# Kernel optimization log

Measured on AMD Instinct MI355X. Metric: run time of the kernel, lower is better.

Reference implementation:

```python
import jax, jax.numpy as jnp
import numpy as np

B, T, HID, H, DH, K = 2, 1024, 1024, 16, 64, 4
ROPE_BASE = 10000.0
EPS = 1e-6


def _causal_dwconv(x, w, b):
    # x: (B, T, C); w: (C, 1, K) depthwise; causal left-pad K-1, then SiLU
    xc = jnp.transpose(x, (0, 2, 1))  # (B, C, T)
    y = jax.lax.conv_general_dilated(
        xc, w, window_strides=(1,), padding=[(K - 1, 0)],
        dimension_numbers=('NCH', 'OIH', 'NCH'), feature_group_count=xc.shape[1])
    y = y + b[None, :, None]
    return jax.nn.silu(jnp.transpose(y, (0, 2, 1)))


def _rope(x, cos, sin):
    # x: (B, T, H, D); cos/sin: (T, D) with emb = cat(freqs, freqs)
    c = cos[None, :, None, :]
    s = sin[None, :, None, :]
    x1, x2 = x[..., ::2], x[..., 1::2]
    return jnp.concatenate(
        [x1 * c[..., ::2] - x2 * s[..., ::2],
         x1 * s[..., ::2] + x2 * c[..., ::2]], axis=-1)


def _delta_rule(q, k, v, alpha, beta, D_param):
    # q,k,v: (B,T,H,DH); alpha,beta: (B,T,H)
    # S_t = alpha_t * (I - beta_t k_t k_t^T) S_{t-1} + beta_t k_t v_t^T
    # o_t  = q_t^T S_t-1-style readout + D * (q.k) * v   (matches torch einsum 'bhd,bhde->bhe')
    qs = jnp.moveaxis(q, 1, 0).astype(jnp.float32)  # (T,B,H,DH)
    ks = jnp.moveaxis(k, 1, 0).astype(jnp.float32)
    vs = jnp.moveaxis(v, 1, 0).astype(jnp.float32)
    als = jnp.moveaxis(alpha, 1, 0).astype(jnp.float32)  # (T,B,H)
    bes = jnp.moveaxis(beta, 1, 0).astype(jnp.float32)

    def step(S, inp):
        qt, kt, vt, at, bt = inp
        ot = jnp.einsum('bhd,bhde->bhe', qt, S)
        ot = ot + D_param[None, :, None] * jnp.sum(qt * kt, -1, keepdims=True) * vt
        kS = jnp.einsum('bhd,bhde->bhe', kt, S)  # k^T S
        at_ = at[..., None, None]
        bt_ = bt[..., None, None]
        S_new = at_ * (S - bt_ * kt[..., :, None] * kS[..., None, :]) \
                + bt_ * kt[..., :, None] * vt[..., None, :]
        return S_new, ot

    S0 = jnp.zeros((q.shape[0], H, DH, DH), jnp.float32)
    _, outs = jax.lax.scan(step, S0, (qs, ks, vs, als, bes))
    return jnp.moveaxis(outs, 0, 1)  # (B,T,H,DH)


def _forward(x, Wq, Wk, Wv, Wg, Wo, bw, bb, gkw, gkb,
             qcw, qcb, kcw, kcb, vcw, vcb, A_log, D_param, dt_bias, onorm_w):
    Bb, Tt, _ = x.shape
    q = _causal_dwconv(x @ Wq, qcw, qcb).reshape(Bb, Tt, H, DH)
    k = _causal_dwconv(x @ Wk, kcw, kcb).reshape(Bb, Tt, H, DH)
    v = _causal_dwconv(x @ Wv, vcw, vcb).reshape(Bb, Tt, H, DH)

    # RoPE (computed on the fly, fp32)
    t = jnp.arange(Tt, dtype=jnp.float32)
    inv_freq = 1.0 / (ROPE_BASE ** (jnp.arange(0, DH, 2, dtype=jnp.float32) / DH))
    freqs = jnp.outer(t, inv_freq)
    emb = jnp.concatenate([freqs, freqs], -1)
    cos, sin = jnp.cos(emb), jnp.sin(emb)
    q = _rope(q, cos, sin)
    k = _rope(k, cos, sin)

    # L2-normalize q/k (delta-net stability, NOT softmax)
    q = q * jax.lax.rsqrt(jnp.sum(q * q, -1, keepdims=True) + EPS)
    k = k * jax.lax.rsqrt(jnp.sum(k * k, -1, keepdims=True) + EPS)

    beta = jax.nn.sigmoid(x @ bw + bb)  # (B,T,H) writing strength
    alpha = jnp.exp(-jnp.exp(A_log) * jax.nn.softplus(x @ gkw + gkb + dt_bias))  # (B,T,H) decay

    o = _delta_rule(q, k, v, alpha, beta, D_param)  # (B,T,H,DH)

    # gated RMSNorm output: g * silu(RMSNorm(o))
    g = (x @ Wg).reshape(Bb, Tt, H, DH)
    on = o * jax.lax.rsqrt(jnp.mean(o * o, -1, keepdims=True) + EPS) * onorm_w
    o = g * jax.nn.silu(on)
    return o.reshape(Bb, Tt, H * DH) @ Wo


def setup_inputs() -> dict:
    key = jax.random.key(0)
    ks = jax.random.split(key, 20)
    w = lambda i, shape, s=0.02: (jax.random.normal(ks[i], shape, jnp.float32) * s)
    return {
        'x': jax.random.normal(ks[0], (B, T, HID), jnp.float32),
        'Wq': w(1, (HID, H * DH)), 'Wk': w(2, (HID, H * DH)),
        'Wv': w(3, (HID, H * DH)), 'Wg': w(4, (HID, H * DH)),
        'Wo': w(5, (H * DH, HID)),
        'bw': w(6, (HID, H)), 'bb': jnp.zeros((H,), jnp.float32),
        'gkw': w(7, (HID, H)), 'gkb': jnp.zeros((H,), jnp.float32),
        'qcw': w(8, (H * DH, 1, K), 0.3), 'qcb': jnp.zeros((H * DH,), jnp.float32),
        'kcw': w(9, (H * DH, 1, K), 0.3), 'kcb': jnp.zeros((H * DH,), jnp.float32),
        'vcw': w(10, (H * DH, 1, K), 0.3), 'vcb': jnp.zeros((H * DH,), jnp.float32),
        'A_log': jnp.log(jax.random.uniform(ks[11], (H,), jnp.float32, 1.0, 16.0)),
        'D_param': jnp.ones((H,), jnp.float32),
        'dt_bias': jax.random.uniform(ks[12], (H,), jnp.float32, -0.01, 0.01),
        'onorm_w': jnp.ones((DH,), jnp.float32),
    }


def reference(x, Wq, Wk, Wv, Wg, Wo, bw, bb, gkw, gkb,
              qcw, qcb, kcw, kcb, vcw, vcb, A_log, D_param, dt_bias, onorm_w):
    return _forward(x, Wq, Wk, Wv, Wg, Wo, bw, bb, gkw, gkb,
                    qcw, qcb, kcw, kcb, vcw, vcb, A_log, D_param, dt_bias, onorm_w)
```

## Files before the change

kernel.cpp:

```cpp
#include <hip/hip_runtime.h>
#include <hip/hip_bf16.h>
#include <cstdint>

#define T_LEN 1024
#define HIDN  1024
#define NH    16
#define DHD   64

typedef __bf16 bf16x8 __attribute__((ext_vector_type(8)));
typedef float  f32x4  __attribute__((ext_vector_type(4)));

__global__ __launch_bounds__(256) void k_tobf16_split(const float* __restrict__ in,
                                                      __bf16* __restrict__ hi,
                                                      __bf16* __restrict__ lo, int n8) {
  int i = blockIdx.x * 256 + threadIdx.x;
  if (i >= n8) return;
  const float4* p = (const float4*)in + (size_t)i * 2;
  float4 a = p[0], b = p[1];
  float v[8] = {a.x, a.y, a.z, a.w, b.x, b.y, b.z, b.w};
  union { __bf16 h[8]; uint4 u; } ph, pl;
#pragma unroll
  for (int j = 0; j < 8; j++) {
    __bf16 h = (__bf16)v[j];
    ph.h[j] = h;
    pl.h[j] = (__bf16)(v[j] - (float)h);
  }
  ((uint4*)hi)[i] = ph.u;
  ((uint4*)lo)[i] = pl.u;
}

__global__ __launch_bounds__(256) void k_transp_split(
    const float* __restrict__ W0, const float* __restrict__ W1,
    const float* __restrict__ W2, const float* __restrict__ W3,
    const float* __restrict__ W4,
    __bf16* __restrict__ H0, __bf16* __restrict__ H1, __bf16* __restrict__ H2,
    __bf16* __restrict__ H3, __bf16* __restrict__ H4,
    __bf16* __restrict__ L0, __bf16* __restrict__ L1, __bf16* __restrict__ L2,
    __bf16* __restrict__ L3, __bf16* __restrict__ L4) {
  const float* W; __bf16* Th; __bf16* Tl;
  switch (blockIdx.z) {
    case 0: W = W0; Th = H0; Tl = L0; break;
    case 1: W = W1; Th = H1; Tl = L1; break;
    case 2: W = W2; Th = H2; Tl = L2; break;
    case 3: W = W3; Th = H3; Tl = L3; break;
    default: W = W4; Th = H4; Tl = L4; break;
  }
  __shared__ float tile[64][65];
  int tid = threadIdx.x;
  int r0 = tid >> 4;
  int c0 = (tid & 15) * 4;
  int kbase = blockIdx.y * 64, nbase = blockIdx.x * 64;
#pragma unroll
  for (int rr = 0; rr < 4; rr++) {
    int r = r0 + rr * 16;
    float4 v = *(const float4*)(W + (size_t)(kbase + r) * 1024 + nbase + c0);
    tile[r][c0 + 0] = v.x; tile[r][c0 + 1] = v.y;
    tile[r][c0 + 2] = v.z; tile[r][c0 + 3] = v.w;
  }
  __syncthreads();
#pragma unroll
  for (int rr = 0; rr < 4; rr++) {
    int n = r0 + rr * 16;
    union { __bf16 h[4]; unsigned long long u; } ph, pl;
#pragma unroll
    for (int j = 0; j < 4; j++) {
      float v = tile[c0 + j][n];
      __bf16 h = (__bf16)v;
      ph.h[j] = h;
      pl.h[j] = (__bf16)(v - (float)h);
    }
    *(unsigned long long*)(Th + (size_t)(nbase + n) * 1024 + kbase + c0) = ph.u;
    *(unsigned long long*)(Tl + (size_t)(nbase + n) * 1024 + kbase + c0) = pl.u;
  }
}

#define LDT 40
__global__ __launch_bounds__(256) void k_gemm3(
    const __bf16* __restrict__ Ah, const __bf16* __restrict__ Al,
    const __bf16* __restrict__ Bh0, const __bf16* __restrict__ Bh1,
    const __bf16* __restrict__ Bh2, const __bf16* __restrict__ Bh3,
    const __bf16* __restrict__ Bl0, const __bf16* __restrict__ Bl1,
    const __bf16* __restrict__ Bl2, const __bf16* __restrict__ Bl3,
    float* __restrict__ C0, float* __restrict__ C1,
    float* __restrict__ C2, float* __restrict__ C3,
    int Kdim, int Ncols) {
  const __bf16* Bh; const __bf16* Bl; float* C;
  switch (blockIdx.z) {
    case 0: Bh = Bh0; Bl = Bl0; C = C0; break;
    case 1: Bh = Bh1; Bl = Bl1; C = C1; break;
    case 2: Bh = Bh2; Bl = Bl2; C = C2; break;
    default: Bh = Bh3; Bl = Bl3; C = C3; break;
  }
  __shared__ __bf16 Ash[128 * LDT];
  __shared__ __bf16 Asl[128 * LDT];
  __shared__ __bf16 Bsh[128 * LDT];
  __shared__ __bf16 Bsl[128 * LDT];
  const int tid = threadIdx.x;
  const int lane = tid & 63;
  const int wave = tid >> 6;
  const int wr = wave >> 1, wc = wave & 1;
  const int rowA0 = blockIdx.y * 128;
  const int colB0 = blockIdx.x * 128;
  const int sseg = tid & 3;
  const int srow0 = tid >> 2;
  const int srow1 = srow0 + 64;

  f32x4 acc[4][4] = {};

  for (int k0 = 0; k0 < Kdim; k0 += 32) {
    size_t a0 = (size_t)(rowA0 + srow0) * Kdim + k0 + sseg * 8;
    size_t a1 = (size_t)(rowA0 + srow1) * Kdim + k0 + sseg * 8;
    size_t b0 = (size_t)(colB0 + srow0) * Kdim + k0 + sseg * 8;
    size_t b1 = (size_t)(colB0 + srow1) * Kdim + k0 + sseg * 8;
    uint4 rah0 = *(const uint4*)(Ah + a0);
    uint4 rah1 = *(const uint4*)(Ah + a1);
    uint4 ral0 = *(const uint4*)(Al + a0);
    uint4 ral1 = *(const uint4*)(Al + a1);
    uint4 rbh0 = *(const uint4*)(Bh + b0);
    uint4 rbh1 = *(const uint4*)(Bh + b1);
    uint4 rbl0 = *(const uint4*)(Bl + b0);
    uint4 rbl1 = *(const uint4*)(Bl + b1);
    __syncthreads();
    *(uint4*)&Ash[srow0 * LDT + sseg * 8] = rah0;
    *(uint4*)&Ash[srow1 * LDT + sseg * 8] = rah1;
    *(uint4*)&Asl[srow0 * LDT + sseg * 8] = ral0;
    *(uint4*)&Asl[srow1 * LDT + sseg * 8] = ral1;
    *(uint4*)&Bsh[srow0 * LDT + sseg * 8] = rbh0;
    *(uint4*)&Bsh[srow1 * LDT + sseg * 8] = rbh1;
    *(uint4*)&Bsl[srow0 * LDT + sseg * 8] = rbl0;
    *(uint4*)&Bsl[srow1 * LDT + sseg * 8] = rbl1;
    __syncthreads();
    bf16x8 afh[4], afl[4], bfh[4], bfl[4];
#pragma unroll
    for (int mi = 0; mi < 4; mi++) {
      int off = (wr * 64 + mi * 16 + (lane & 15)) * LDT + (lane >> 4) * 8;
      afh[mi] = *(const bf16x8*)&Ash[off];
      afl[mi] = *(const bf16x8*)&Asl[off];
    }
#pragma unroll
    for (int ni = 0; ni < 4; ni++) {
      int off = (wc * 64 + ni * 16 + (lane & 15)) * LDT + (lane >> 4) * 8;
      bfh[ni] = *(const bf16x8*)&Bsh[off];
      bfl[ni] = *(const bf16x8*)&Bsl[off];
    }
#pragma unroll
    for (int mi = 0; mi < 4; mi++)
#pragma unroll
      for (int ni = 0; ni < 4; ni++) {
        acc[mi][ni] = __builtin_amdgcn_mfma_f32_16x16x32_bf16(afh[mi], bfh[ni], acc[mi][ni], 0, 0, 0);
        acc[mi][ni] = __builtin_amdgcn_mfma_f32_16x16x32_bf16(afl[mi], bfh[ni], acc[mi][ni], 0, 0, 0);
        acc[mi][ni] = __builtin_amdgcn_mfma_f32_16x16x32_bf16(afh[mi], bfl[ni], acc[mi][ni], 0, 0, 0);
      }
  }
#pragma unroll
  for (int mi = 0; mi < 4; mi++)
#pragma unroll
    for (int ni = 0; ni < 4; ni++) {
      int col = colB0 + wc * 64 + ni * 16 + (lane & 15);
#pragma unroll
      for (int r = 0; r < 4; r++) {
        int row = rowA0 + wr * 64 + mi * 16 + (lane >> 4) * 4 + r;
        C[(size_t)row * Ncols + col] = acc[mi][ni][r];
      }
    }
}

__global__ __launch_bounds__(256) void k_gates(
    const float* __restrict__ x, const float* __restrict__ bw,
    const float* __restrict__ bb, const float* __restrict__ gkw,
    const float* __restrict__ gkb, const float* __restrict__ A_log,
    const float* __restrict__ dt_bias,
    float* __restrict__ alphaB, float* __restrict__ betaB) {
  const int bt = blockIdx.x;
  const int tid = threadIdx.x;
  const int h = tid & 15;
  const int chunk = tid >> 4;
  const float* xr = x + (size_t)bt * HIDN;
  float d1 = 0.f, d2 = 0.f;
#pragma unroll 8
  for (int j = 0; j < 64; j++) {
    int k = chunk * 64 + j;
    float xv = xr[k];
    d1 += xv * bw[k * 16 + h];
    d2 += xv * gkw[k * 16 + h];
  }
  __shared__ float p1[16][16], p2[16][16];
  p1[chunk][h] = d1; p2[chunk][h] = d2;
  __syncthreads();
  if (tid < 16) {
    float s1 = 0.f, s2 = 0.f;
#pragma unroll
    for (int c = 0; c < 16; c++) { s1 += p1[c][tid]; s2 += p2[c][tid]; }
    float beta = 1.f / (1.f + expf(-(s1 + bb[tid])));
    float z = s2 + gkb[tid] + dt_bias[tid];
    float sp = fmaxf(z, 0.f) + log1pf(expf(-fabsf(z)));
    float alpha = expf(-expf(A_log[tid]) * sp);
    alphaB[(size_t)bt * 16 + tid] = alpha;
    betaB[(size_t)bt * 16 + tid] = beta;
  }
}

__global__ __launch_bounds__(256) void k_rope_table(float* __restrict__ ct,
                                                    float* __restrict__ st) {
  int idx = blockIdx.x * 256 + threadIdx.x;
  if (idx >= T_LEN * 32) return;
  int t = idx >> 5, i = idx & 31;
  int m = 2 * (i & 15);
  float f = expf(-(float)m * (9.210340371976184f / 32.f));
  float ang = (float)t * f;
  ct[idx] = cosf(ang);
  st[idx] = sinf(ang);
}

__global__ __launch_bounds__(256) void k_conv(
    const float* __restrict__ in0, const float* __restrict__ in1,
    const float* __restrict__ in2,
    const float* __restrict__ w0, const float* __restrict__ w1,
    const float* __restrict__ w2,
    const float* __restrict__ b0, const float* __restrict__ b1,
    const float* __restrict__ b2,
    float* __restrict__ o0, float* __restrict__ o1, float* __restrict__ o2) {
  const int tensor = blockIdx.y;
  const float* in; const float* w; const float* bias; float* out;
  switch (tensor) {
    case 0: in = in0; w = w0; bias = b0; out = o0; break;
    case 1: in = in1; w = w1; bias = b1; out = o1; break;
    default: in = in2; w = w2; bias = b2; out = o2; break;
  }
  int idx = blockIdx.x * 256 + threadIdx.x;
  int c = idx & 1023;
  int bt = idx >> 10;
  int t = bt & 1023, b = bt >> 10;
  float4 wc4 = *(const float4*)(w + (size_t)c * 4);
  const float* col = in + ((size_t)b * 1024) * 1024 + c;
  float xm3 = (t >= 3) ? col[(size_t)(t - 3) * 1024] : 0.f;
  float xm2 = (t >= 2) ? col[(size_t)(t - 2) * 1024] : 0.f;
  float xm1 = (t >= 1) ? col[(size_t)(t - 1) * 1024] : 0.f;
  float x0 = col[(size_t)t * 1024];
  float acc = bias[c] + wc4.x * xm3 + wc4.y * xm2 + wc4.z * xm1 + wc4.w * x0;
  float y = acc / (1.f + expf(-acc));
  if (tensor < 2) {
    out[(size_t)bt * 1024 + c] = y;
  } else {
    int h = c >> 6, d = c & 63;
    out[(((size_t)(b * 16 + h)) * 1024 + t) * 64 + d] = y;
  }
}

__global__ __launch_bounds__(256) void k_ropenorm(
    const float* __restrict__ qc, const float* __restrict__ kc,
    const float* __restrict__ ct, const float* __restrict__ st,
    const float* __restrict__ alphaB, const float* __restrict__ betaB,
    const float* __restrict__ Dp,
    float* __restrict__ qr, float* __restrict__ kr, float4* __restrict__ aux) {
  int widx = blockIdx.x * 4 + (threadIdx.x >> 6);
  int lane = threadIdx.x & 63;
  int h = widx & 15;
  int bt = widx >> 4;
  int t = bt & 1023, b = bt >> 10;
  const float* qrow = qc + (size_t)bt * 1024 + h * 64;
  const float* krow = kc + (size_t)bt * 1024 + h * 64;
  int i = lane & 31;
  float cv = ct[t * 32 + i], sv = st[t * 32 + i];
  float q1 = qrow[2 * i], q2 = qrow[2 * i + 1];
  float k1 = krow[2 * i], k2 = krow[2 * i + 1];
  float qo = (lane < 32) ? (q1 * cv - q2 * sv) : (q1 * sv + q2 * cv);
  float ko = (lane < 32) ? (k1 * cv - k2 * sv) : (k1 * sv + k2 * cv);
  float qs = qo * qo, ks2 = ko * ko;
#pragma unroll
  for (int m = 1; m < 64; m <<= 1) { qs += __shfl_xor(qs, m); ks2 += __shfl_xor(ks2, m); }
  float qn = qo * rsqrtf(qs + 1e-6f);
  float kn = ko * rsqrtf(ks2 + 1e-6f);
  float dq = qn * kn;
#pragma unroll
  for (int m = 1; m < 64; m <<= 1) dq += __shfl_xor(dq, m);
  size_t obase = ((size_t)(b * 16 + h) * 1024 + t) * 64;
  qr[obase + lane] = qn;
  kr[obase + lane] = kn;
  if (lane == 0) {
    float alpha = alphaB[(size_t)bt * 16 + h];
    float beta = betaB[(size_t)bt * 16 + h];
    aux[(size_t)(b * 16 + h) * 1024 + t] = make_float4(alpha, beta, alpha * beta, Dp[h] * dq);
  }
}

__global__ __launch_bounds__(128) void k_scanA(
    const float* __restrict__ qr, const float* __restrict__ kr,
    const float* __restrict__ vr, const float4* __restrict__ aux,
    float* __restrict__ O1, float* __restrict__ AcF,
    float* __restrict__ BcTF, float* __restrict__ QeffF,
    float* __restrict__ gcF) {
  const int bid = blockIdx.x;
  const int bh = bid >> 4, c = bid & 15;
  const int t0 = c * 64;
  const int tid = threadIdx.x;
  const int w = tid >> 6, lane = tid & 63;
  const float* qB = qr + (size_t)bh * 65536 + (size_t)t0 * 64;
  const float* kB = kr + (size_t)bh * 65536 + (size_t)t0 * 64;
  const float* vB = vr + (size_t)bh * 65536 + (size_t)t0 * 64;
  const float4* auxB = aux + (size_t)bh * T_LEN + t0;

  __shared__ __bf16 q_b[64 * 72];
  __shared__ __bf16 k_b[64 * 72];
  __shared__ __bf16 kT_b[64 * 72];
  __shared__ __bf16 C_b[64 * 72];
  __shared__ __bf16 U0T[64 * 72];
  __shared__ __bf16 WT[64 * 72];
  __shared__ float  vS[64 * 64];
  __shared__ float  MTf[64 * 68];
  __shared__ float  lgS[64], pvS[64], beS[64], awS[64], enS[64];

  if (w == 0) {
    float4 a4 = auxB[lane];
    float lg = logf(a4.x);
#pragma unroll
    for (int off = 1; off < 64; off <<= 1) {
      float tv = __shfl_up(lg, off);
      if (lane >= off) lg += tv;
    }
    float pv = __shfl_up(lg, 1);
    if (lane == 0) pv = 0.f;
    float lgTot = __shfl(lg, 63);
    lgS[lane] = lg; pvS[lane] = pv; beS[lane] = a4.y; awS[lane] = a4.w;
    enS[lane] = expf(lgTot - lg);
    if (lane == 0) gcF[bid] = expf(lgTot);
  }
#pragma unroll
  for (int p = 0; p < 4; p++) {
    int s = p * 128 + tid;
    int row = s >> 3, col8 = s & 7;
    const float* gq = qB + (size_t)row * 64 + col8 * 8;
    const float* gk = kB + (size_t)row * 64 + col8 * 8;
    const float* gv = vB + (size_t)row * 64 + col8 * 8;
    float4 q0 = *(const float4*)gq, q1 = *(const float4*)(gq + 4);
    float4 k0 = *(const float4*)gk, k1 = *(const float4*)(gk + 4);
    float4 v0 = *(const float4*)gv, v1 = *(const float4*)(gv + 4);
    union { __bf16 h[8]; uint4 u; } pq, pk;
    pq.h[0] = (__bf16)q0.x; pq.h[1] = (__bf16)q0.y; pq.h[2] = (__bf16)q0.z; pq.h[3] = (__bf16)q0.w;
    pq.h[4] = (__bf16)q1.x; pq.h[5] = (__bf16)q1.y; pq.h[6] = (__bf16)q1.z; pq.h[7] = (__bf16)q1.w;
    pk.h[0] = (__bf16)k0.x; pk.h[1] = (__bf16)k0.y; pk.h[2] = (__bf16)k0.z; pk.h[3] = (__bf16)k0.w;
    pk.h[4] = (__bf16)k1.x; pk.h[5] = (__bf16)k1.y; pk.h[6] = (__bf16)k1.z; pk.h[7] = (__bf16)k1.w;
    *(uint4*)&q_b[row * 72 + col8 * 8] = pq.u;
    *(uint4*)&k_b[row * 72 + col8 * 8] = pk.u;
    *(float4*)&vS[row * 64 + col8 * 8] = v0;
    *(float4*)&vS[row * 64 + col8 * 8 + 4] = v1;
  }
  __syncthreads();

#pragma unroll
  for (int mm = 0; mm < 2; mm++) {
    int mi = w * 2 + mm;
#pragma unroll
    for (int ni = 0; ni < 4; ni++) {
      f32x4 akk = {0.f, 0.f, 0.f, 0.f};
      f32x4 aqk = {0.f, 0.f, 0.f, 0.f};
#pragma unroll
      for (int ks = 0; ks < 2; ks++) {
        bf16x8 fa_k = *(const bf16x8*)&k_b[(mi * 16 + (lane & 15)) * 72 + ks * 32 + (lane >> 4) * 8];
        bf16x8 fa_q = *(const bf16x8*)&q_b[(mi * 16 + (lane & 15)) * 72 + ks * 32 + (lane >> 4) * 8];
        bf16x8 fb_k = *(const bf16x8*)&k_b[(ni * 16 + (lane & 15)) * 72 + ks * 32 + (lane >> 4) * 8];
        akk = __builtin_amdgcn_mfma_f32_16x16x32_bf16(fa_k, fb_k, akk, 0, 0, 0);
        aqk = __builtin_amdgcn_mfma_f32_16x16x32_bf16(fa_q, fb_k, aqk, 0, 0, 0);
      }
#pragma unroll
      for (int r = 0; r < 4; r++) {
        int row = mi * 16 + (lane >> 4) * 4 + r;
        int col = ni * 16 + (lane & 15);
        float mt = 0.f, cv = 0.f;
        if (row > col) {
          mt = beS[row] * expf(lgS[row] - lgS[col]) * akk[r];
          cv = expf(pvS[row] - lgS[col]) * aqk[r];
        }
        MTf[col * 68 + row] = mt;
        C_b[row * 72 + col] = (__bf16)cv;
      }
    }
  }
  __syncthreads();

  if (w == 1) {
#pragma unroll
    for (int t8 = 0; t8 < 8; t8++) {
      union { __bf16 h[8]; uint4 u; } pt;
#pragma unroll
      for (int q = 0; q < 8; q++) {
        int t = t8 * 8 + q;
        pt.h[q] = (__bf16)((float)k_b[t * 72 + lane] * enS[t]);
      }
      *(uint4*)&kT_b[lane * 72 + t8 * 8] = pt.u;
    }
  }

  {
    float u[64];
    if (w == 0) {
#pragma unroll
      for (int j = 0; j < 64; j++) u[j] = beS[j] * vS[j * 64 + lane];
    } else {
#pragma unroll
      for (int j = 0; j < 64; j++) u[j] = beS[j] * expf(lgS[j]) * (float)k_b[j * 72 + lane];
    }
    __bf16* dst = (w == 0) ? U0T : WT;
#pragma unroll
    for (int j = 0; j < 64; j++) {
      dst[lane * 72 + j] = (__bf16)u[j];
      float uj = u[j];
#pragma unroll
      for (int g = (j >> 4); g < 4; g++) {
#pragma unroll
        for (int q4 = 0; q4 < 4; q4++) {
          const float4 m4 = *(const float4*)&MTf[j * 68 + g * 16 + q4 * 4];
          u[g * 16 + q4 * 4 + 0] -= m4.x * uj;
          u[g * 16 + q4 * 4 + 1] -= m4.y * uj;
          u[g * 16 + q4 * 4 + 2] -= m4.z * uj;
          u[g * 16 + q4 * 4 + 3] -= m4.w * uj;
        }
      }
    }
  }
  __syncthreads();

  size_t cb = (size_t)bid * 4096;
  if (w == 0) {
#pragma unroll
    for (int mi = 0; mi < 4; mi++)
#pragma unroll
      for (int ni = 0; ni < 4; ni++) {
        f32x4 ab = {0.f, 0.f, 0.f, 0.f};
        f32x4 aa = {0.f, 0.f, 0.f, 0.f};
#pragma unroll
        for (int ks = 0; ks < 2; ks++) {
          int aoff = (mi * 16 + (lane & 15)) * 72 + ks * 32 + (lane >> 4) * 8;
          int boff = (ni * 16 + (lane & 15)) * 72 + ks * 32 + (lane >> 4) * 8;
          bf16x8 fu = *(const bf16x8*)&U0T[aoff];
          bf16x8 fkm = *(const bf16x8*)&kT_b[aoff];
          bf16x8 fkn = *(const bf16x8*)&kT_b[boff];
          bf16x8 fw = *(const bf16x8*)&WT[boff];
          ab = __builtin_amdgcn_mfma_f32_16x16x32_bf16(fu, fkn, ab, 0, 0, 0);
          aa = __builtin_amdgcn_mfma_f32_16x16x32_bf16(fkm, fw, aa, 0, 0, 0);
        }
#pragma unroll
        for (int r = 0; r < 4; r++) {
          int row = mi * 16 + (lane >> 4) * 4 + r;
          int col = ni * 16 + (lane & 15);
          BcTF[cb + row * 64 + col] = ab[r];
          AcF[cb + row * 64 + col] = aa[r];
        }
      }
  } else {
#pragma unroll
    for (int mi = 0; mi < 4; mi++)
#pragma unroll
      for (int ni = 0; ni < 4; ni++) {
        f32x4 ao = {0.f, 0.f, 0.f, 0.f};
        f32x4 ac = {0.f, 0.f, 0.f, 0.f};
#pragma unroll
        for (int ks = 0; ks < 2; ks++) {
          int aoff = (mi * 16 + (lane & 15)) * 72 + ks * 32 + (lane >> 4) * 8;
          int boff = (ni * 16 + (lane & 15)) * 72 + ks * 32 + (lane >> 4) * 8;
          bf16x8 fc = *(const bf16x8*)&C_b[aoff];
          bf16x8 fu = *(const bf16x8*)&U0T[boff];
          bf16x8 fw = *(const bf16x8*)&WT[boff];
          ao = __builtin_amdgcn_mfma_f32_16x16x32_bf16(fc, fu, ao, 0, 0, 0);
          ac = __builtin_amdgcn_mfma_f32_16x16x32_bf16(fc, fw, ac, 0, 0, 0);
        }
#pragma unroll
        for (int r = 0; r < 4; r++) {
          int t = mi * 16 + (lane >> 4) * 4 + r;
          int col = ni * 16 + (lane & 15);
          O1[(size_t)bh * 65536 + (size_t)(t0 + t) * 64 + col] =
              ao[r] + awS[t] * vS[t * 64 + col];
          QeffF[cb + t * 64 + col] = expf(pvS[t]) * (float)q_b[t * 72 + col] - ac[r];
        }
      }
  }
}

__global__ __launch_bounds__(256) void k_scanB(
    const float* __restrict__ AcF, const float* __restrict__ BcTF,
    const float* __restrict__ gcF, float* __restrict__ S0TF) {
  const int bh = blockIdx.x;
  const int tid = threadIdx.x;
  const int w = tid >> 6, lane = tid & 63;
  const int er = tid >> 2, seg = (tid & 3) * 16;
  __shared__ float STf[64 * 68];
  __shared__ __bf16 Sh[64 * 72], Sl[64 * 72], Ac_b[64 * 72];
#pragma unroll
  for (int i = 0; i < 4; i++)
    *(float4*)&STf[er * 68 + seg + i * 4] = make_float4(0.f, 0.f, 0.f, 0.f);
  __syncthreads();

  for (int c = 0; c < 16; c++) {
    size_t cb = (size_t)(bh * 16 + c) * 4096;
#pragma unroll
    for (int i = 0; i < 4; i++) {
      float4 s = *(const float4*)&STf[er * 68 + seg + i * 4];
      *(float4*)&S0TF[cb + er * 64 + seg + i * 4] = s;
      union { __bf16 h[4]; unsigned long long u; } ph, pl;
      float sv[4] = {s.x, s.y, s.z, s.w};
#pragma unroll
      for (int q = 0; q < 4; q++) {
        __bf16 hv = (__bf16)sv[q];
        ph.h[q] = hv;
        pl.h[q] = (__bf16)(sv[q] - (float)hv);
      }
      *(unsigned long long*)&Sh[er * 72 + seg + i * 4] = ph.u;
      *(unsigned long long*)&Sl[er * 72 + seg + i * 4] = pl.u;
    }
#pragma unroll
    for (int i = 0; i < 4; i++) {
      float4 a = *(const float4*)&AcF[cb + er * 64 + seg + i * 4];
      union { __bf16 h[4]; unsigned long long u; } pa;
      pa.h[0] = (__bf16)a.x; pa.h[1] = (__bf16)a.y;
      pa.h[2] = (__bf16)a.z; pa.h[3] = (__bf16)a.w;
      *(unsigned long long*)&Ac_b[er * 72 + seg + i * 4] = pa.u;
    }
    float gC = gcF[bh * 16 + c];
    __syncthreads();

    f32x4 acc[4];
#pragma unroll
    for (int ni = 0; ni < 4; ni++) {
      acc[ni] = (f32x4){0.f, 0.f, 0.f, 0.f};
#pragma unroll
      for (int ks = 0; ks < 2; ks++) {
        int aoff = (w * 16 + (lane & 15)) * 72 + ks * 32 + (lane >> 4) * 8;
        int boff = (ni * 16 + (lane & 15)) * 72 + ks * 32 + (lane >> 4) * 8;
        bf16x8 ah = *(const bf16x8*)&Sh[aoff];
        bf16x8 al = *(const bf16x8*)&Sl[aoff];
        bf16x8 bb = *(const bf16x8*)&Ac_b[boff];
        acc[ni] = __builtin_amdgcn_mfma_f32_16x16x32_bf16(ah, bb, acc[ni], 0, 0, 0);
        acc[ni] = __builtin_amdgcn_mfma_f32_16x16x32_bf16(al, bb, acc[ni], 0, 0, 0);
      }
    }
#pragma unroll
    for (int ni = 0; ni < 4; ni++)
#pragma unroll
      for (int r = 0; r < 4; r++) {
        int e = w * 16 + (lane >> 4) * 4 + r;
        int d = ni * 16 + (lane & 15);
        float bct = BcTF[cb + e * 64 + d];
        STf[e * 68 + d] = gC * STf[e * 68 + d] - acc[ni][r] + bct;
      }
    __syncthreads();
  }
}

__global__ __launch_bounds__(256) void k_scanC(
    const float* __restrict__ S0TF, const float* __restrict__ QeffF,
    float* __restrict__ obuf) {
  const int bid = blockIdx.x;
  const int bh = bid >> 4, c = bid & 15, t0 = c * 64;
  const int tid = threadIdx.x;
  const int w = tid >> 6, lane = tid & 63;
  const int er = tid >> 2, seg = (tid & 3) * 16;
  size_t cb = (size_t)bid * 4096;
  __shared__ __bf16 Sh[64 * 72], Sl[64 * 72], Qb[64 * 72];
#pragma unroll
  for (int i = 0; i < 4; i++) {
    float4 s = *(const float4*)&S0TF[cb + er * 64 + seg + i * 4];
    union { __bf16 h[4]; unsigned long long u; } ph, pl;
    float sv[4] = {s.x, s.y, s.z, s.w};
#pragma unroll
    for (int q = 0; q < 4; q++) {
      __bf16 hv = (__bf16)sv[q];
      ph.h[q] = hv;
      pl.h[q] = (__bf16)(sv[q] - (float)hv);
    }
    *(unsigned long long*)&Sh[er * 72 + seg + i * 4] = ph.u;
    *(unsigned long long*)&Sl[er * 72 + seg + i * 4] = pl.u;
    float4 qq = *(const float4*)&QeffF[cb + er * 64 + seg + i * 4];
    union { __bf16 h[4]; unsigned long long u; } pq;
    pq.h[0] = (__bf16)qq.x; pq.h[1] = (__bf16)qq.y;
    pq.h[2] = (__bf16)qq.z; pq.h[3] = (__bf16)qq.w;
    *(unsigned long long*)&Qb[er * 72 + seg + i * 4] = pq.u;
  }
  __syncthreads();
#pragma unroll
  for (int ni = 0; ni < 4; ni++) {
    f32x4 acc = {0.f, 0.f, 0.f, 0.f};
#pragma unroll
    for (int ks = 0; ks < 2; ks++) {
      int aoff = (w * 16 + (lane & 15)) * 72 + ks * 32 + (lane >> 4) * 8;
      int boff = (ni * 16 + (lane & 15)) * 72 + ks * 32 + (lane >> 4) * 8;
      bf16x8 fq = *(const bf16x8*)&Qb[aoff];
      bf16x8 sh = *(const bf16x8*)&Sh[boff];
      bf16x8 sl = *(const bf16x8*)&Sl[boff];
      acc = __builtin_amdgcn_mfma_f32_16x16x32_bf16(fq, sh, acc, 0, 0, 0);
      acc = __builtin_amdgcn_mfma_f32_16x16x32_bf16(fq, sl, acc, 0, 0, 0);
    }
#pragma unroll
    for (int r = 0; r < 4; r++) {
      int t = w * 16 + (lane >> 4) * 4 + r;
      int e = ni * 16 + (lane & 15);
      size_t oi = (size_t)bh * 65536 + (size_t)(t0 + t) * 64 + e;
      obuf[oi] += acc[r];
    }
  }
}

__global__ __launch_bounds__(256) void k_outnorm(
    const float* __restrict__ obuf, const float* __restrict__ g,
    const float* __restrict__ onw, __bf16* __restrict__ rh,
    __bf16* __restrict__ rl) {
  int widx = blockIdx.x * 4 + (threadIdx.x >> 6);
  int lane = threadIdx.x & 63;
  int h = widx & 15, bt = widx >> 4;
  int t = bt & 1023, b = bt >> 10;
  float ov = obuf[(((size_t)(b * 16 + h)) * 1024 + t) * 64 + lane];
  float ss = ov * ov;
#pragma unroll
  for (int m = 1; m < 64; m <<= 1) ss += __shfl_xor(ss, m);
  float on = ov * rsqrtf(ss * (1.f / 64.f) + 1e-6f) * onw[lane];
  float sil = on / (1.f + expf(-on));
  float gv = g[(size_t)bt * 1024 + h * 64 + lane];
  float r = gv * sil;
  __bf16 hv = (__bf16)r;
  rh[(size_t)bt * 1024 + h * 64 + lane] = hv;
  rl[(size_t)bt * 1024 + h * 64 + lane] = (__bf16)(r - (float)hv);
}

extern "C" void kernel_launch(void* const* d_in, const int* in_sizes, int n_in,
                              void* d_out, int out_size, void* d_ws, size_t ws_size,
                              hipStream_t stream) {
  (void)in_sizes; (void)n_in; (void)out_size; (void)ws_size;
  const float* x    = (const float*)d_in[0];
  const float* Wq   = (const float*)d_in[1];
  const float* Wk   = (const float*)d_in[2];
  const float* Wv   = (const float*)d_in[3];
  const float* Wg   = (const float*)d_in[4];
  const float* Wo   = (const float*)d_in[5];
  const float* bw   = (const float*)d_in[6];
  const float* bb   = (const float*)d_in[7];
  const float* gkw  = (const float*)d_in[8];
  const float* gkb  = (const float*)d_in[9];
  const float* qcw  = (const float*)d_in[10];
  const float* qcb  = (const float*)d_in[11];
  const float* kcw  = (const float*)d_in[12];
  const float* kcb  = (const float*)d_in[13];
  const float* vcw  = (const float*)d_in[14];
  const float* vcb  = (const float*)d_in[15];
  const float* A_log= (const float*)d_in[16];
  const float* Dp   = (const float*)d_in[17];
  const float* dtb  = (const float*)d_in[18];
  const float* onw  = (const float*)d_in[19];

  char* ws = (char*)d_ws;
  const size_t MB = 1024 * 1024;
  __bf16* xb_h = (__bf16*)(ws + 0);
  __bf16* xb_l = (__bf16*)(ws + 4 * MB);
  __bf16* Wq_h = (__bf16*)(ws + 8 * MB);
  __bf16* Wq_l = (__bf16*)(ws + 10 * MB);
  __bf16* Wk_h = (__bf16*)(ws + 12 * MB);
  __bf16* Wk_l = (__bf16*)(ws + 14 * MB);
  __bf16* Wv_h = (__bf16*)(ws + 16 * MB);
  __bf16* Wv_l = (__bf16*)(ws + 18 * MB);
  __bf16* Wg_h = (__bf16*)(ws + 20 * MB);
  __bf16* Wg_l = (__bf16*)(ws + 22 * MB);
  __bf16* Wo_h = (__bf16*)(ws + 24 * MB);
  __bf16* Wo_l = (__bf16*)(ws + 26 * MB);
  float* q_pre = (float*)(ws + 28 * MB);
  float* k_pre = (float*)(ws + 36 * MB);
  float* v_pre = (float*)(ws + 44 * MB);
  float* g_buf = (float*)(ws + 52 * MB);
  float* qc    = (float*)(ws + 0);
  float* kc    = (float*)(ws + 8 * MB);
  float* vr    = (float*)(ws + 16 * MB);
  float* qrb   = q_pre;
  float* krb   = k_pre;
  float* obuf  = v_pre;
  __bf16* r_h  = (__bf16*)(ws + 0);
  __bf16* r_l  = (__bf16*)(ws + 4 * MB);
  float* AcF   = (float*)(ws + 0);
  float* BcTF  = (float*)(ws + 8 * MB);
  float* S0TF  = (float*)(ws + 28 * MB);
  float* QeffF = (float*)(ws + 61 * MB);
  float* gcF   = (float*)(ws + 69 * MB);
  float* alphaB = (float*)(ws + 60 * MB);
  float* betaB  = (float*)(ws + 60 * MB + 128 * 1024);
  float4* aux   = (float4*)(ws + 60 * MB + 256 * 1024);
  float* ct     = (float*)(ws + 60 * MB + 768 * 1024);
  float* st     = (float*)(ws + 60 * MB + 896 * 1024);
  float* out    = (float*)d_out;

  k_tobf16_split<<<1024, 256, 0, stream>>>(x, xb_h, xb_l, 262144);
  k_transp_split<<<dim3(16, 16, 5), 256, 0, stream>>>(
      Wq, Wk, Wv, Wg, Wo,
      Wq_h, Wk_h, Wv_h, Wg_h, Wo_h,
      Wq_l, Wk_l, Wv_l, Wg_l, Wo_l);
  k_rope_table<<<128, 256, 0, stream>>>(ct, st);
  k_gates<<<2048, 256, 0, stream>>>(x, bw, bb, gkw, gkb, A_log, dtb, alphaB, betaB);
  k_gemm3<<<dim3(8, 16, 4), 256, 0, stream>>>(
      xb_h, xb_l,
      Wq_h, Wk_h, Wv_h, Wg_h,
      Wq_l, Wk_l, Wv_l, Wg_l,
      q_pre, k_pre, v_pre, g_buf, 1024, 1024);
  k_conv<<<dim3(8192, 3), 256, 0, stream>>>(q_pre, k_pre, v_pre, qcw, kcw, vcw,
                                            qcb, kcb, vcb, qc, kc, vr);
  k_ropenorm<<<8192, 256, 0, stream>>>(qc, kc, ct, st, alphaB, betaB, Dp, qrb, krb, aux);
  k_scanA<<<512, 128, 0, stream>>>(qrb, krb, vr, aux, obuf, AcF, BcTF, QeffF, gcF);
  k_scanB<<<32, 256, 0, stream>>>(AcF, BcTF, gcF, S0TF);
  k_scanC<<<512, 256, 0, stream>>>(S0TF, QeffF, obuf);
  k_outnorm<<<8192, 256, 0, stream>>>(obuf, g_buf, onw, r_h, r_l);
  k_gemm3<<<dim3(8, 16, 1), 256, 0, stream>>>(
      r_h, r_l,
      Wo_h, Wo_h, Wo_h, Wo_h,
      Wo_l, Wo_l, Wo_l, Wo_l,
      out, out, out, out, 1024, 1024);
}
```

Before: 343.7 us.

## Fuse conv/rope/norm, scanC/outnorm, and bf16 split into GEMM A-load

```diff
diff --git a/kernel.cpp b/kernel.cpp
--- a/kernel.cpp
+++ b/kernel.cpp
@@ -10,23 +10,16 @@
 typedef __bf16 bf16x8 __attribute__((ext_vector_type(8)));
 typedef float  f32x4  __attribute__((ext_vector_type(4)));
 
-__global__ __launch_bounds__(256) void k_tobf16_split(const float* __restrict__ in,
-                                                      __bf16* __restrict__ hi,
-                                                      __bf16* __restrict__ lo, int n8) {
-  int i = blockIdx.x * 256 + threadIdx.x;
-  if (i >= n8) return;
-  const float4* p = (const float4*)in + (size_t)i * 2;
-  float4 a = p[0], b = p[1];
-  float v[8] = {a.x, a.y, a.z, a.w, b.x, b.y, b.z, b.w};
+__device__ inline void split8(float4 x0, float4 x1, uint4& hi, uint4& lo) {
   union { __bf16 h[8]; uint4 u; } ph, pl;
+  float v[8] = {x0.x, x0.y, x0.z, x0.w, x1.x, x1.y, x1.z, x1.w};
 #pragma unroll
   for (int j = 0; j < 8; j++) {
     __bf16 h = (__bf16)v[j];
     ph.h[j] = h;
     pl.h[j] = (__bf16)(v[j] - (float)h);
   }
-  ((uint4*)hi)[i] = ph.u;
-  ((uint4*)lo)[i] = pl.u;
+  hi = ph.u; lo = pl.u;
 }
 
 __global__ __launch_bounds__(256) void k_transp_split(
@@ -75,8 +68,8 @@
 }
 
 #define LDT 40
-__global__ __launch_bounds__(256) void k_gemm3(
-    const __bf16* __restrict__ Ah, const __bf16* __restrict__ Al,
+__global__ __launch_bounds__(256) void k_gemm3f(
+    const float* __restrict__ Af,
     const __bf16* __restrict__ Bh0, const __bf16* __restrict__ Bh1,
     const __bf16* __restrict__ Bh2, const __bf16* __restrict__ Bh3,
     const __bf16* __restrict__ Bl0, const __bf16* __restrict__ Bl1,
@@ -112,14 +105,17 @@
     size_t a1 = (size_t)(rowA0 + srow1) * Kdim + k0 + sseg * 8;
     size_t b0 = (size_t)(colB0 + srow0) * Kdim + k0 + sseg * 8;
     size_t b1 = (size_t)(colB0 + srow1) * Kdim + k0 + sseg * 8;
-    uint4 rah0 = *(const uint4*)(Ah + a0);
-    uint4 rah1 = *(const uint4*)(Ah + a1);
-    uint4 ral0 = *(const uint4*)(Al + a0);
-    uint4 ral1 = *(const uint4*)(Al + a1);
+    float4 a00 = *(const float4*)(Af + a0);
+    float4 a01 = *(const float4*)(Af + a0 + 4);
+    float4 a10 = *(const float4*)(Af + a1);
+    float4 a11 = *(const float4*)(Af + a1 + 4);
     uint4 rbh0 = *(const uint4*)(Bh + b0);
     uint4 rbh1 = *(const uint4*)(Bh + b1);
     uint4 rbl0 = *(const uint4*)(Bl + b0);
     uint4 rbl1 = *(const uint4*)(Bl + b1);
+    uint4 rah0, ral0, rah1, ral1;
+    split8(a00, a01, rah0, ral0);
+    split8(a10, a11, rah1, ral1);
     __syncthreads();
     *(uint4*)&Ash[srow0 * LDT + sseg * 8] = rah0;
     *(uint4*)&Ash[srow1 * LDT + sseg * 8] = rah1;
@@ -200,72 +196,65 @@
   }
 }
 
-__global__ __launch_bounds__(256) void k_rope_table(float* __restrict__ ct,
-                                                    float* __restrict__ st) {
-  int idx = blockIdx.x * 256 + threadIdx.x;
-  if (idx >= T_LEN * 32) return;
-  int t = idx >> 5, i = idx & 31;
-  int m = 2 * (i & 15);
-  float f = expf(-(float)m * (9.210340371976184f / 32.f));
-  float ang = (float)t * f;
-  ct[idx] = cosf(ang);
-  st[idx] = sinf(ang);
-}
-
-__global__ __launch_bounds__(256) void k_conv(
-    const float* __restrict__ in0, const float* __restrict__ in1,
-    const float* __restrict__ in2,
-    const float* __restrict__ w0, const float* __restrict__ w1,
-    const float* __restrict__ w2,
-    const float* __restrict__ b0, const float* __restrict__ b1,
-    const float* __restrict__ b2,
-    float* __restrict__ o0, float* __restrict__ o1, float* __restrict__ o2) {
-  const int tensor = blockIdx.y;
-  const float* in; const float* w; const float* bias; float* out;
-  switch (tensor) {
-    case 0: in = in0; w = w0; bias = b0; out = o0; break;
-    case 1: in = in1; w = w1; bias = b1; out = o1; break;
-    default: in = in2; w = w2; bias = b2; out = o2; break;
-  }
-  int idx = blockIdx.x * 256 + threadIdx.x;
-  int c = idx & 1023;
-  int bt = idx >> 10;
-  int t = bt & 1023, b = bt >> 10;
-  float4 wc4 = *(const float4*)(w + (size_t)c * 4);
-  const float* col = in + ((size_t)b * 1024) * 1024 + c;
-  float xm3 = (t >= 3) ? col[(size_t)(t - 3) * 1024] : 0.f;
-  float xm2 = (t >= 2) ? col[(size_t)(t - 2) * 1024] : 0.f;
-  float xm1 = (t >= 1) ? col[(size_t)(t - 1) * 1024] : 0.f;
-  float x0 = col[(size_t)t * 1024];
-  float acc = bias[c] + wc4.x * xm3 + wc4.y * xm2 + wc4.z * xm1 + wc4.w * x0;
-  float y = acc / (1.f + expf(-acc));
-  if (tensor < 2) {
-    out[(size_t)bt * 1024 + c] = y;
-  } else {
-    int h = c >> 6, d = c & 63;
-    out[(((size_t)(b * 16 + h)) * 1024 + t) * 64 + d] = y;
-  }
-}
-
-__global__ __launch_bounds__(256) void k_ropenorm(
-    const float* __restrict__ qc, const float* __restrict__ kc,
-    const float* __restrict__ ct, const float* __restrict__ st,
+__global__ __launch_bounds__(256) void k_cra(
+    const float* __restrict__ qp, const float* __restrict__ kp,
+    const float* __restrict__ vp,
+    const float* __restrict__ qcw, const float* __restrict__ qcb,
+    const float* __restrict__ kcw, const float* __restrict__ kcb,
+    const float* __restrict__ vcw, const float* __restrict__ vcb,
     const float* __restrict__ alphaB, const float* __restrict__ betaB,
     const float* __restrict__ Dp,
-    float* __restrict__ qr, float* __restrict__ kr, float4* __restrict__ aux) {
+    float* __restrict__ qr, float* __restrict__ kr, float* __restrict__ vr,
+    float4* __restrict__ aux) {
   int widx = blockIdx.x * 4 + (threadIdx.x >> 6);
   int lane = threadIdx.x & 63;
   int h = widx & 15;
   int bt = widx >> 4;
   int t = bt & 1023, b = bt >> 10;
-  const float* qrow = qc + (size_t)bt * 1024 + h * 64;
-  const float* krow = kc + (size_t)bt * 1024 + h * 64;
+  int c = h * 64 + lane;
+  size_t colbase = ((size_t)b * 1024) * 1024 + c;
+
+  float4 wq = *(const float4*)(qcw + (size_t)c * 4);
+  float4 wk = *(const float4*)(kcw + (size_t)c * 4);
+  float4 wv = *(const float4*)(vcw + (size_t)c * 4);
+  float aq = qcb[c], ak = kcb[c], av = vcb[c];
+  {
+    float x0 = qp[colbase + (size_t)t * 1024];
+    float y0 = kp[colbase + (size_t)t * 1024];
+    float z0 = vp[colbase + (size_t)t * 1024];
+    aq += wq.w * x0; ak += wk.w * y0; av += wv.w * z0;
+    if (t >= 1) {
+      float x1 = qp[colbase + (size_t)(t - 1) * 1024];
+      float y1 = kp[colbase + (size_t)(t - 1) * 1024];
+      float z1 = vp[colbase + (size_t)(t - 1) * 1024];
+      aq += wq.z * x1; ak += wk.z * y1; av += wv.z * z1;
+    }
+    if (t >= 2) {
+      float x2 = qp[colbase + (size_t)(t - 2) * 1024];
+      float y2 = kp[colbase + (size_t)(t - 2) * 1024];
+      float z2 = vp[colbase + (size_t)(t - 2) * 1024];
+      aq += wq.y * x2; ak += wk.y * y2; av += wv.y * z2;
+    }
+    if (t >= 3) {
+      float x3 = qp[colbase + (size_t)(t - 3) * 1024];
+      float y3 = kp[colbase + (size_t)(t - 3) * 1024];
+      float z3 = vp[colbase + (size_t)(t - 3) * 1024];
+      aq += wq.x * x3; ak += wk.x * y3; av += wv.x * z3;
+    }
+  }
+  float yq = aq / (1.f + expf(-aq));
+  float yk = ak / (1.f + expf(-ak));
+  float yv = av / (1.f + expf(-av));
+
   int i = lane & 31;
-  float cv = ct[t * 32 + i], sv = st[t * 32 + i];
-  float q1 = qrow[2 * i], q2 = qrow[2 * i + 1];
-  float k1 = krow[2 * i], k2 = krow[2 * i + 1];
+  float fr = expf(-(float)(2 * (i & 15)) * (9.210340371976184f / 32.f));
+  float ang = (float)t * fr;
+  float cv = cosf(ang), sv = sinf(ang);
+  float q1 = __shfl(yq, 2 * i), q2 = __shfl(yq, 2 * i + 1);
+  float k1 = __shfl(yk, 2 * i), k2 = __shfl(yk, 2 * i + 1);
   float qo = (lane < 32) ? (q1 * cv - q2 * sv) : (q1 * sv + q2 * cv);
   float ko = (lane < 32) ? (k1 * cv - k2 * sv) : (k1 * sv + k2 * cv);
+
   float qs = qo * qo, ks2 = ko * ko;
 #pragma unroll
   for (int m = 1; m < 64; m <<= 1) { qs += __shfl_xor(qs, m); ks2 += __shfl_xor(ks2, m); }
@@ -277,6 +266,7 @@
   size_t obase = ((size_t)(b * 16 + h) * 1024 + t) * 64;
   qr[obase + lane] = qn;
   kr[obase + lane] = kn;
+  vr[obase + lane] = yv;
   if (lane == 0) {
     float alpha = alphaB[(size_t)bt * 16 + h];
     float beta = betaB[(size_t)bt * 16 + h];
@@ -490,33 +480,65 @@
     *(float4*)&STf[er * 68 + seg + i * 4] = make_float4(0.f, 0.f, 0.f, 0.f);
   __syncthreads();
 
+  size_t cbase = (size_t)bh * 16 * 4096;
+  float4 acR[4];
+  float bctR[16];
+#pragma unroll
+  for (int i = 0; i < 4; i++)
+    acR[i] = *(const float4*)&AcF[cbase + er * 64 + seg + i * 4];
+#pragma unroll
+  for (int r = 0; r < 4; r++)
+#pragma unroll
+    for (int ni = 0; ni < 4; ni++) {
+      int e = w * 16 + (lane >> 4) * 4 + r;
+      int d = ni * 16 + (lane & 15);
+      bctR[r * 4 + ni] = BcTF[cbase + e * 64 + d];
+    }
+
   for (int c = 0; c < 16; c++) {
-    size_t cb = (size_t)(bh * 16 + c) * 4096;
+    size_t cb = cbase + (size_t)c * 4096;
 #pragma unroll
     for (int i = 0; i < 4; i++) {
       float4 s = *(const float4*)&STf[er * 68 + seg + i * 4];
       *(float4*)&S0TF[cb + er * 64 + seg + i * 4] = s;
-      union { __bf16 h[4]; unsigned long long u; } ph, pl;
+      union { __bf16 h[4]; unsigned long long u; } ph, pl, pa;
       float sv[4] = {s.x, s.y, s.z, s.w};
+      float av[4] = {acR[i].x, acR[i].y, acR[i].z, acR[i].w};
 #pragma unroll
       for (int q = 0; q < 4; q++) {
         __bf16 hv = (__bf16)sv[q];
         ph.h[q] = hv;
         pl.h[q] = (__bf16)(sv[q] - (float)hv);
+        pa.h[q] = (__bf16)av[q];
       }
       *(unsigned long long*)&Sh[er * 72 + seg + i * 4] = ph.u;
       *(unsigned long long*)&Sl[er * 72 + seg + i * 4] = pl.u;
-    }
-#pragma unroll
-    for (int i = 0; i < 4; i++) {
-      float4 a = *(const float4*)&AcF[cb + er * 64 + seg + i * 4];
-      union { __bf16 h[4]; unsigned long long u; } pa;
-      pa.h[0] = (__bf16)a.x; pa.h[1] = (__bf16)a.y;
-      pa.h[2] = (__bf16)a.z; pa.h[3] = (__bf16)a.w;
       *(unsigned long long*)&Ac_b[er * 72 + seg + i * 4] = pa.u;
     }
     float gC = gcF[bh * 16 + c];
     __syncthreads();
+
+    float4 acN[4];
+    float bctN[16];
+    if (c < 15) {
+      size_t nb = cb + 4096;
+#pragma unroll
+      for (int i = 0; i < 4; i++)
+        acN[i] = *(const float4*)&AcF[nb + er * 64 + seg + i * 4];
+#pragma unroll
+      for (int r = 0; r < 4; r++)
+#pragma unroll
+        for (int ni = 0; ni < 4; ni++) {
+          int e = w * 16 + (lane >> 4) * 4 + r;
+          int d = ni * 16 + (lane & 15);
+          bctN[r * 4 + ni] = BcTF[nb + e * 64 + d];
+        }
+    } else {
+#pragma unroll
+      for (int i = 0; i < 4; i++) acN[i] = acR[i];
+#pragma unroll
+      for (int j = 0; j < 16; j++) bctN[j] = bctR[j];
+    }
 
     f32x4 acc[4];
 #pragma unroll
@@ -539,18 +561,23 @@
       for (int r = 0; r < 4; r++) {
         int e = w * 16 + (lane >> 4) * 4 + r;
         int d = ni * 16 + (lane & 15);
-        float bct = BcTF[cb + e * 64 + d];
-        STf[e * 68 + d] = gC * STf[e * 68 + d] - acc[ni][r] + bct;
+        STf[e * 68 + d] = gC * STf[e * 68 + d] - acc[ni][r] + bctR[r * 4 + ni];
       }
     __syncthreads();
-  }
-}
-
-__global__ __launch_bounds__(256) void k_scanC(
+#pragma unroll
+    for (int i = 0; i < 4; i++) acR[i] = acN[i];
+#pragma unroll
+    for (int j = 0; j < 16; j++) bctR[j] = bctN[j];
+  }
+}
+
+__global__ __launch_bounds__(256) void k_scanCn(
     const float* __restrict__ S0TF, const float* __restrict__ QeffF,
-    float* __restrict__ obuf) {
+    const float* __restrict__ obuf, const float* __restrict__ g,
+    const float* __restrict__ onw, float* __restrict__ robuf) {
   const int bid = blockIdx.x;
-  const int bh = bid >> 4, c = bid & 15, t0 = c * 64;
+  const int bh = bid >> 4, c = bid & 15, t0c = c * 64;
+  const int b = bh >> 4, h = bh & 15;
   const int tid = threadIdx.x;
   const int w = tid >> 6, lane = tid & 63;
   const int er = tid >> 2, seg = (tid & 3) * 16;
@@ -576,9 +603,10 @@
     *(unsigned long long*)&Qb[er * 72 + seg + i * 4] = pq.u;
   }
   __syncthreads();
+  f32x4 acc[4];
 #pragma unroll
   for (int ni = 0; ni < 4; ni++) {
-    f32x4 acc = {0.f, 0.f, 0.f, 0.f};
+    acc[ni] = (f32x4){0.f, 0.f, 0.f, 0.f};
 #pragma unroll
     for (int ks = 0; ks < 2; ks++) {
       int aoff = (w * 16 + (lane & 15)) * 72 + ks * 32 + (lane >> 4) * 8;
@@ -586,38 +614,37 @@
       bf16x8 fq = *(const bf16x8*)&Qb[aoff];
       bf16x8 sh = *(const bf16x8*)&Sh[boff];
       bf16x8 sl = *(const bf16x8*)&Sl[boff];
-      acc = __builtin_amdgcn_mfma_f32_16x16x32_bf16(fq, sh, acc, 0, 0, 0);
-      acc = __builtin_amdgcn_mfma_f32_16x16x32_bf16(fq, sl, acc, 0, 0, 0);
-    }
-#pragma unroll
-    for (int r = 0; r < 4; r++) {
-      int t = w * 16 + (lane >> 4) * 4 + r;
+      acc[ni] = __builtin_amdgcn_mfma_f32_16x16x32_bf16(fq, sh, acc[ni], 0, 0, 0);
+      acc[ni] = __builtin_amdgcn_mfma_f32_16x16x32_bf16(fq, sl, acc[ni], 0, 0, 0);
+    }
+  }
+  float onwv[4];
+#pragma unroll
+  for (int ni = 0; ni < 4; ni++) onwv[ni] = onw[ni * 16 + (lane & 15)];
+#pragma unroll
+  for (int r = 0; r < 4; r++) {
+    int t = w * 16 + (lane >> 4) * 4 + r;
+    float o[4];
+#pragma unroll
+    for (int ni = 0; ni < 4; ni++) {
       int e = ni * 16 + (lane & 15);
-      size_t oi = (size_t)bh * 65536 + (size_t)(t0 + t) * 64 + e;
-      obuf[oi] += acc[r];
-    }
-  }
-}
-
-__global__ __launch_bounds__(256) void k_outnorm(
-    const float* __restrict__ obuf, const float* __restrict__ g,
-    const float* __restrict__ onw, __bf16* __restrict__ rh,
-    __bf16* __restrict__ rl) {
-  int widx = blockIdx.x * 4 + (threadIdx.x >> 6);
-  int lane = threadIdx.x & 63;
-  int h = widx & 15, bt = widx >> 4;
-  int t = bt & 1023, b = bt >> 10;
-  float ov = obuf[(((size_t)(b * 16 + h)) * 1024 + t) * 64 + lane];
-  float ss = ov * ov;
-#pragma unroll
-  for (int m = 1; m < 64; m <<= 1) ss += __shfl_xor(ss, m);
-  float on = ov * rsqrtf(ss * (1.f / 64.f) + 1e-6f) * onw[lane];
-  float sil = on / (1.f + expf(-on));
-  float gv = g[(size_t)bt * 1024 + h * 64 + lane];
-  float r = gv * sil;
-  __bf16 hv = (__bf16)r;
-  rh[(size_t)bt * 1024 + h * 64 + lane] = hv;
-  rl[(size_t)bt * 1024 + h * 64 + lane] = (__bf16)(r - (float)hv);
+      o[ni] = obuf[(size_t)bh * 65536 + (size_t)(t0c + t) * 64 + e] + acc[ni][r];
+    }
+    float ss = o[0] * o[0] + o[1] * o[1] + o[2] * o[2] + o[3] * o[3];
+    ss += __shfl_xor(ss, 1);
+    ss += __shfl_xor(ss, 2);
+    ss += __shfl_xor(ss, 4);
+    ss += __shfl_xor(ss, 8);
+    float rinv = rsqrtf(ss * (1.f / 64.f) + 1e-6f);
+    size_t gbase = ((size_t)(b * 1024 + t0c + t)) * 1024 + h * 64;
+#pragma unroll
+    for (int ni = 0; ni < 4; ni++) {
+      int e = ni * 16 + (lane & 15);
+      float on = o[ni] * rinv * onwv[ni];
+      float sil = on / (1.f + expf(-on));
+      robuf[gbase + e] = g[gbase + e] * sil;
+    }
+  }
 }
 
 extern "C" void kernel_launch(void* const* d_in, const int* in_sizes, int n_in,
@@ -647,8 +674,6 @@
 
   char* ws = (char*)d_ws;
   const size_t MB = 1024 * 1024;
-  __bf16* xb_h = (__bf16*)(ws + 0);
-  __bf16* xb_l = (__bf16*)(ws + 4 * MB);
   __bf16* Wq_h = (__bf16*)(ws + 8 * MB);
   __bf16* Wq_l = (__bf16*)(ws + 10 * MB);
   __bf16* Wk_h = (__bf16*)(ws + 12 * MB);
@@ -663,47 +688,39 @@
   float* k_pre = (float*)(ws + 36 * MB);
   float* v_pre = (float*)(ws + 44 * MB);
   float* g_buf = (float*)(ws + 52 * MB);
-  float* qc    = (float*)(ws + 0);
-  float* kc    = (float*)(ws + 8 * MB);
+  float* qrb   = (float*)(ws + 0);
+  float* krb   = (float*)(ws + 8 * MB);
   float* vr    = (float*)(ws + 16 * MB);
-  float* qrb   = q_pre;
-  float* krb   = k_pre;
   float* obuf  = v_pre;
-  __bf16* r_h  = (__bf16*)(ws + 0);
-  __bf16* r_l  = (__bf16*)(ws + 4 * MB);
-  float* AcF   = (float*)(ws + 0);
-  float* BcTF  = (float*)(ws + 8 * MB);
-  float* S0TF  = (float*)(ws + 28 * MB);
-  float* QeffF = (float*)(ws + 61 * MB);
-  float* gcF   = (float*)(ws + 69 * MB);
+  float* AcF   = (float*)(ws + 28 * MB);
+  float* BcTF  = (float*)(ws + 36 * MB);
+  float* S0TF  = (float*)(ws + 0);
+  float* QeffF = (float*)(ws + 16 * MB);
+  float* robuf = (float*)(ws + 8 * MB);
   float* alphaB = (float*)(ws + 60 * MB);
   float* betaB  = (float*)(ws + 60 * MB + 128 * 1024);
   float4* aux   = (float4*)(ws + 60 * MB + 256 * 1024);
-  float* ct     = (float*)(ws + 60 * MB + 768 * 1024);
-  float* st     = (float*)(ws + 60 * MB + 896 * 1024);
+  float* gcF    = (float*)(ws + 60 * MB + 768 * 1024);
   float* out    = (float*)d_out;
 
-  k_tobf16_split<<<1024, 256, 0, stream>>>(x, xb_h, xb_l, 262144);
   k_transp_split<<<dim3(16, 16, 5), 256, 0, stream>>>(
       Wq, Wk, Wv, Wg, Wo,
       Wq_h, Wk_h, Wv_h, Wg_h, Wo_h,
       Wq_l, Wk_l, Wv_l, Wg_l, Wo_l);
-  k_rope_table<<<128, 256, 0, stream>>>(ct, st);
   k_gates<<<2048, 256, 0, stream>>>(x, bw, bb, gkw, gkb, A_log, dtb, alphaB, betaB);
-  k_gemm3<<<dim3(8, 16, 4), 256, 0, stream>>>(
-      xb_h, xb_l,
+  k_gemm3f<<<dim3(8, 16, 4), 256, 0, stream>>>(
+      x,
       Wq_h, Wk_h, Wv_h, Wg_h,
       Wq_l, Wk_l, Wv_l, Wg_l,
       q_pre, k_pre, v_pre, g_buf, 1024, 1024);
-  k_conv<<<dim3(8192, 3), 256, 0, stream>>>(q_pre, k_pre, v_pre, qcw, kcw, vcw,
-                                            qcb, kcb, vcb, qc, kc, vr);
-  k_ropenorm<<<8192, 256, 0, stream>>>(qc, kc, ct, st, alphaB, betaB, Dp, qrb, krb, aux);
+  k_cra<<<8192, 256, 0, stream>>>(q_pre, k_pre, v_pre,
+                                  qcw, qcb, kcw, kcb, vcw, vcb,
+                                  alphaB, betaB, Dp, qrb, krb, vr, aux);
   k_scanA<<<512, 128, 0, stream>>>(qrb, krb, vr, aux, obuf, AcF, BcTF, QeffF, gcF);
   k_scanB<<<32, 256, 0, stream>>>(AcF, BcTF, gcF, S0TF);
-  k_scanC<<<512, 256, 0, stream>>>(S0TF, QeffF, obuf);
-  k_outnorm<<<8192, 256, 0, stream>>>(obuf, g_buf, onw, r_h, r_l);
-  k_gemm3<<<dim3(8, 16, 1), 256, 0, stream>>>(
-      r_h, r_l,
+  k_scanCn<<<512, 256, 0, stream>>>(S0TF, QeffF, obuf, g_buf, onw, robuf);
+  k_gemm3f<<<dim3(8, 16, 1), 256, 0, stream>>>(
+      robuf,
       Wo_h, Wo_h, Wo_h, Wo_h,
       Wo_l, Wo_l, Wo_l, Wo_l,
       out, out, out, out, 1024, 1024);
```

Result: faster. 331.7 us (-3.5%).
